# Kernel tuning notes

Hardware: AMD Instinct MI355X
Metric: run time of the kernel (lower is better)

The kernel has to match this reference:

```python
import jax, jax.numpy as jnp
import numpy as np

N = 100000   # nodes
E = 1600000  # edges (avg degree 16)
D = 64       # feature / hidden / embedding dim
OUT = 2
NEG_SLOPE = 0.2


def setup_inputs() -> dict:
    key = jax.random.key(0)
    ks = jax.random.split(key, 12)
    s = 1.0 / np.sqrt(D)
    return {
        "x": jax.random.normal(ks[0], (N, D), dtype=jnp.float32),
        "edge_index": jax.random.randint(ks[1], (2, E), 0, N, dtype=jnp.int64),
        "Wl": jax.random.normal(ks[2], (3, D, D), dtype=jnp.float32) * s,
        "bl": jnp.zeros((3, D), dtype=jnp.float32),
        "Wr": jax.random.normal(ks[3], (3, D, D), dtype=jnp.float32) * s,
        "br": jnp.zeros((3, D), dtype=jnp.float32),
        "att": jax.random.normal(ks[4], (3, D), dtype=jnp.float32) * s,
        "bg": jnp.zeros((3, D), dtype=jnp.float32),
        "Ws": jax.random.normal(ks[5], (3, D, D), dtype=jnp.float32) * s,
        "bs": jnp.zeros((3, D), dtype=jnp.float32),
        "Wout": jax.random.normal(ks[6], (D, OUT), dtype=jnp.float32) * s,
        "bout": jnp.zeros((OUT,), dtype=jnp.float32),
    }


def _gatv2(h, src, dst, Wl, bl, Wr, br, att, bg):
    # GATv2Conv (heads=1, concat, add_self_loops=False):
    #   e_ij = att . LeakyReLU(Wl h_j + Wr h_i); softmax over incoming edges of i;
    #   out_i = sum_j alpha_ij * (Wl h_j) + bias
    xl = h @ Wl + bl                      # [N, D] source transform
    xr = h @ Wr + br                      # [N, D] dest transform
    e = jax.nn.leaky_relu(xl[src] + xr[dst], NEG_SLOPE) @ att  # [E]
    m = jax.ops.segment_max(e, dst, num_segments=N)            # per-dest max
    a = jnp.exp(e - m[dst])                                    # [E]
    denom = jax.ops.segment_sum(a, dst, num_segments=N)        # [N]
    alpha = a / denom[dst]                                     # [E]
    agg = jax.ops.segment_sum(alpha[:, None] * xl[src], dst, num_segments=N)
    return agg + bg                                            # [N, D]


def reference(x, edge_index, Wl, bl, Wr, br, att, bg, Ws, bs, Wout, bout):
    src, dst = edge_index[0], edge_index[1]
    # layer 1: gat1 + skip1, relu (dropout_rate=0 -> identity)
    h = jax.nn.relu(_gatv2(x, src, dst, Wl[0], bl[0], Wr[0], br[0], att[0], bg[0])
                    + x @ Ws[0] + bs[0])
    # middle layer
    h = jax.nn.relu(_gatv2(h, src, dst, Wl[1], bl[1], Wr[1], br[1], att[1], bg[1])
                    + h @ Ws[1] + bs[1])
    # last gat layer: no relu after
    h = _gatv2(h, src, dst, Wl[2], bl[2], Wr[2], br[2], att[2], bg[2]) + h @ Ws[2] + bs[2]
    return h @ Wout + bout
```

## Files before the change

kernel.cpp:

```cpp
#include <hip/hip_runtime.h>
#include <stdint.h>

#define NN 100000
#define EE 1600000
#define DD 64
#define NBUCK 391
#define SCWG 200
#define SCCHUNK 8000

using short8 = __attribute__((ext_vector_type(8))) short;
using f32x4  = __attribute__((ext_vector_type(4))) float;
using f2     = __attribute__((ext_vector_type(2))) float;


__device__ __forceinline__ unsigned short bf16_rne(float f) {
    unsigned int u = __float_as_uint(f);
    unsigned int r = (u + 0x7FFFu + ((u >> 16) & 1u)) >> 16;
    return (unsigned short)r;
}
__device__ __forceinline__ float bf16_to_f32(unsigned short h) {
    return __uint_as_float(((unsigned int)h) << 16);
}


__global__ void bucket_hist(const int* __restrict__ dst, int* __restrict__ bhist) {
    __shared__ int h[NBUCK];
    int t = threadIdx.x;
    for (int b = t; b < NBUCK; b += 256) h[b] = 0;
    __syncthreads();
    int start = blockIdx.x * SCCHUNK;
    int endi = min(start + SCCHUNK, EE);
    for (int e = start + t; e < endi; e += 256)
        atomicAdd(&h[dst[e] >> 8], 1);
    __syncthreads();
    for (int b = t; b < NBUCK; b += 256)
        if (h[b]) atomicAdd(&bhist[b], h[b]);
}

__global__ void bucket_scan(const int* __restrict__ bhist, int* __restrict__ bbase,
                            int* __restrict__ bcursor, int* __restrict__ offsets) {
    __shared__ int s[512];
    int t = threadIdx.x;
    int v = (t < NBUCK) ? bhist[t] : 0;
    s[t] = v;
    __syncthreads();
    for (int off = 1; off < 512; off <<= 1) {
        int a = (t >= off) ? s[t - off] : 0;
        __syncthreads();
        s[t] += a;
        __syncthreads();
    }
    if (t < NBUCK) { int excl = s[t] - v; bbase[t] = excl; bcursor[t] = excl; }
    if (t == 0) { bbase[NBUCK] = EE; offsets[NN] = EE; }
}

__global__ void bucket_scatter(const int* __restrict__ src, const int* __restrict__ dst,
                               int* __restrict__ bcursor, int2* __restrict__ bedges) {
    __shared__ int cnt[NBUCK];
    __shared__ int lcur[NBUCK];
    int t = threadIdx.x;
    for (int b = t; b < NBUCK; b += 256) cnt[b] = 0;
    __syncthreads();
    int start = blockIdx.x * SCCHUNK;
    int endi = min(start + SCCHUNK, EE);
    for (int e = start + t; e < endi; e += 256)
        atomicAdd(&cnt[dst[e] >> 8], 1);
    __syncthreads();
    for (int b = t; b < NBUCK; b += 256) {
        int c = cnt[b];
        lcur[b] = c ? atomicAdd(&bcursor[b], c) : 0;
    }
    __syncthreads();
    for (int e = start + t; e < endi; e += 256) {
        int d = dst[e];
        int pos = atomicAdd(&lcur[d >> 8], 1);
        int2 v; v.x = d; v.y = src[e];
        bedges[pos] = v;
    }
}

__global__ void bucket_csr(const int2* __restrict__ bedges, const int* __restrict__ bbase,
                           int* __restrict__ offsets, int* __restrict__ csr) {
    __shared__ int ncnt[256];
    __shared__ int lofs[256];
    int b = blockIdx.x;
    int t = threadIdx.x;
    int beg = bbase[b], endb = bbase[b + 1];
    ncnt[t] = 0;
    __syncthreads();
    for (int e = beg + t; e < endb; e += 256)
        atomicAdd(&ncnt[bedges[e].x & 255], 1);
    __syncthreads();
    int v = ncnt[t];
    lofs[t] = v;
    __syncthreads();
    for (int off = 1; off < 256; off <<= 1) {
        int a = (t >= off) ? lofs[t - off] : 0;
        __syncthreads();
        lofs[t] += a;
        __syncthreads();
    }
    int excl = lofs[t] - v;
    int node = b * 256 + t;
    if (node < NN) offsets[node] = beg + excl;
    __syncthreads();
    ncnt[t] = beg + excl;
    __syncthreads();
    for (int e = beg + t; e < endb; e += 256) {
        int2 ed = bedges[e];
        int pos = atomicAdd(&ncnt[ed.x & 255], 1);
        csr[pos] = ed.y;
    }
}


__global__ void conv_w(const float* __restrict__ Wl, const float* __restrict__ Wr,
                       const float* __restrict__ Ws,
                       unsigned short* __restrict__ Wt_hi, unsigned short* __restrict__ Wt_lo) {
    int e = blockIdx.x * 256 + threadIdx.x;
    if (e >= 9 * 4096) return;
    int mat = e >> 12;
    int r   = e & 4095;
    int k   = r >> 6, n = r & 63;
    int L = mat / 3, j = mat % 3;
    const float* W = (j == 0) ? Wl : ((j == 1) ? Wr : Ws);
    float v = W[L * 4096 + k * 64 + n];
    unsigned short hi = bf16_rne(v);
    unsigned short lo = bf16_rne(v - bf16_to_f32(hi));
    Wt_hi[mat * 4096 + n * 64 + k] = hi;
    Wt_lo[mat * 4096 + n * 64 + k] = lo;
}


__global__ void conv_x(const float* __restrict__ x,
                       unsigned short* __restrict__ Ahi, unsigned short* __restrict__ Alo) {
    int i = blockIdx.x * 256 + threadIdx.x;
    int total = NN * 16;
    for (; i < total; i += gridDim.x * 256) {
        float4 v = *(const float4*)&x[(size_t)i * 4];
        ushort4 h, l;
        h.x = bf16_rne(v.x); l.x = bf16_rne(v.x - bf16_to_f32(h.x));
        h.y = bf16_rne(v.y); l.y = bf16_rne(v.y - bf16_to_f32(h.y));
        h.z = bf16_rne(v.z); l.z = bf16_rne(v.z - bf16_to_f32(h.z));
        h.w = bf16_rne(v.w); l.w = bf16_rne(v.w - bf16_to_f32(h.w));
        *(ushort4*)&Ahi[(size_t)i * 4] = h;
        *(ushort4*)&Alo[(size_t)i * 4] = l;
    }
}


__global__ __launch_bounds__(256) void gemm_mfma(
    const unsigned short* __restrict__ Ahi, const unsigned short* __restrict__ Alo,
    const unsigned short* __restrict__ Wt_hi, const unsigned short* __restrict__ Wt_lo,
    const float* __restrict__ bl, const float* __restrict__ br, const float* __restrict__ bs,
    float* __restrict__ Xl, float* __restrict__ XRS) {
    int lane = threadIdx.x & 63;
    int wid  = threadIdx.x >> 6;
    int m0 = (blockIdx.x * 4 + wid) * 16;
    if (m0 >= NN) return;

    int arow = m0 + (lane & 15);
    if (arow >= NN) arow = NN - 1;
    int koff = (lane >> 4) * 8;

    const unsigned short* abase = Ahi + (size_t)arow * 64;
    const unsigned short* lbase = Alo + (size_t)arow * 64;
    short8 ahi0 = *(const short8*)(abase + koff);
    short8 ahi1 = *(const short8*)(abase + 32 + koff);
    short8 alo0 = *(const short8*)(lbase + koff);
    short8 alo1 = *(const short8*)(lbase + 32 + koff);

    int col16 = lane & 15;
    int r0 = m0 + ((lane >> 4) << 2);

#pragma unroll
    for (int m = 0; m < 3; m++) {
        const unsigned short* wh = Wt_hi + m * 4096;
        const unsigned short* wl = Wt_lo + m * 4096;
        const float* bias = (m == 0) ? bl : ((m == 1) ? br : bs);
#pragma unroll
        for (int tt = 0; tt < 4; tt++) {
            int ncol = tt * 16 + col16;
            const unsigned short* bh = wh + ncol * 64 + koff;
            const unsigned short* blo = wl + ncol * 64 + koff;
            short8 bhi0 = *(const short8*)bh;
            short8 bhi1 = *(const short8*)(bh + 32);
            short8 blo0 = *(const short8*)blo;
            short8 blo1 = *(const short8*)(blo + 32);

            f32x4 acc = {0.f, 0.f, 0.f, 0.f};
            acc = __builtin_amdgcn_mfma_f32_16x16x32_bf16(ahi0, bhi0, acc, 0, 0, 0);
            acc = __builtin_amdgcn_mfma_f32_16x16x32_bf16(ahi1, bhi1, acc, 0, 0, 0);
            acc = __builtin_amdgcn_mfma_f32_16x16x32_bf16(ahi0, blo0, acc, 0, 0, 0);
            acc = __builtin_amdgcn_mfma_f32_16x16x32_bf16(ahi1, blo1, acc, 0, 0, 0);
            acc = __builtin_amdgcn_mfma_f32_16x16x32_bf16(alo0, bhi0, acc, 0, 0, 0);
            acc = __builtin_amdgcn_mfma_f32_16x16x32_bf16(alo1, bhi1, acc, 0, 0, 0);

            float bb = bias[ncol];
#pragma unroll
            for (int j = 0; j < 4; j++) {
                int row = r0 + j;
                if (row < NN) {
                    float v = acc[j] + bb;
                    if (m == 0)      Xl[(size_t)row * 64 + ncol]        = v;
                    else if (m == 1) XRS[(size_t)row * 128 + ncol]      = v;
                    else             XRS[(size_t)row * 128 + 64 + ncol] = v;
                }
            }
        }
    }
}


__device__ __forceinline__ float group_sum16(float t) {
    t += __int_as_float(__builtin_amdgcn_update_dpp(0, __float_as_int(t), 0xB1, 0xF, 0xF, true));
    t += __int_as_float(__builtin_amdgcn_update_dpp(0, __float_as_int(t), 0x4E, 0xF, 0xF, true));
    t += __int_as_float(__builtin_amdgcn_update_dpp(0, __float_as_int(t), 0x141, 0xF, 0xF, true));
    t += __int_as_float(__builtin_amdgcn_update_dpp(0, __float_as_int(t), 0x140, 0xF, 0xF, true));
    return t;
}

__global__ __launch_bounds__(256) void node_kernel(
    const float* __restrict__ Xl, const float* __restrict__ XRS,
    const int* __restrict__ offsets, const int* __restrict__ csr,
    const float* __restrict__ att, const float* __restrict__ bg,
    unsigned short* __restrict__ houtHi, unsigned short* __restrict__ houtLo, int do_relu,
    const float* __restrict__ Wout, const float* __restrict__ bout,
    float* __restrict__ outp, int do_out) {
    int lane = threadIdx.x & 63;
    int wid  = threadIdx.x >> 6;
    int i = blockIdx.x * 4 + wid;
    if (i >= NN) return;
    int sub = lane & 15;
    int grp = lane >> 4;

    float4 xr4  = *(const float4*)&XRS[(size_t)i * 128 + sub * 4];
    float4 att4 = *(const float4*)&att[sub * 4];
    f2 xr01 = {xr4.x, xr4.y}, xr23 = {xr4.z, xr4.w};
    f2 at01 = {att4.x, att4.y}, at23 = {att4.z, att4.w};

    f2 agg01 = {0.f, 0.f}, agg23 = {0.f, 0.f};
    float denom = 0.f;
    int beg = offsets[i], end = offsets[i + 1];

    for (int j0 = beg; j0 < end; j0 += 8) {
        int jA = j0 + grp, jB = j0 + grp + 4;
        bool vA = jA < end, vB = jB < end;
        int sA = csr[vA ? jA : beg];
        int sB = csr[vB ? jB : beg];
        float4 xA = *(const float4*)&Xl[(size_t)sA * 64 + sub * 4];
        float4 xB = *(const float4*)&Xl[(size_t)sB * 64 + sub * 4];
        f2 xA01 = {xA.x, xA.y}, xA23 = {xA.z, xA.w};
        f2 xB01 = {xB.x, xB.y}, xB23 = {xB.z, xB.w};

        f2 sA01 = xA01 + xr01;
        f2 sA23 = xA23 + xr23;
        f2 sB01 = xB01 + xr01;
        f2 sB23 = xB23 + xr23;
        f2 lA01 = { fmaxf(sA01.x, 0.2f * sA01.x), fmaxf(sA01.y, 0.2f * sA01.y) };
        f2 lA23 = { fmaxf(sA23.x, 0.2f * sA23.x), fmaxf(sA23.y, 0.2f * sA23.y) };
        f2 lB01 = { fmaxf(sB01.x, 0.2f * sB01.x), fmaxf(sB01.y, 0.2f * sB01.y) };
        f2 lB23 = { fmaxf(sB23.x, 0.2f * sB23.x), fmaxf(sB23.y, 0.2f * sB23.y) };

        f2 tAv = lA01 * at01 + lA23 * at23;
        f2 tBv = lB01 * at01 + lB23 * at23;
        float tA = group_sum16(tAv.x + tAv.y);
        float tB = group_sum16(tBv.x + tBv.y);
        float aA = vA ? __expf(tA) : 0.f;
        float aB = vB ? __expf(tB) : 0.f;

        f2 aAv = {aA, aA};
        f2 aBv = {aB, aB};
        agg01 += aAv * xA01 + aBv * xB01;
        agg23 += aAv * xA23 + aBv * xB23;
        denom += aA + aB;
    }

    float aggx = agg01.x, aggy = agg01.y, aggz = agg23.x, aggw = agg23.y;
#pragma unroll
    for (int m = 16; m <= 32; m <<= 1) {
        aggx  += __shfl_xor(aggx, m, 64);
        aggy  += __shfl_xor(aggy, m, 64);
        aggz  += __shfl_xor(aggz, m, 64);
        aggw  += __shfl_xor(aggw, m, 64);
        denom += __shfl_xor(denom, m, 64);
    }

    float inv = (denom > 0.f) ? (1.0f / denom) : 0.f;
    float4 sk4 = *(const float4*)&XRS[(size_t)i * 128 + 64 + sub * 4];
    float4 bg4 = *(const float4*)&bg[sub * 4];
    float4 res;
    res.x = aggx * inv + bg4.x + sk4.x;
    res.y = aggy * inv + bg4.y + sk4.y;
    res.z = aggz * inv + bg4.z + sk4.z;
    res.w = aggw * inv + bg4.w + sk4.w;
    if (do_relu) {
        res.x = fmaxf(res.x, 0.f); res.y = fmaxf(res.y, 0.f);
        res.z = fmaxf(res.z, 0.f); res.w = fmaxf(res.w, 0.f);
    }
    if (do_out) {
        float4 w01 = *(const float4*)&Wout[8 * sub];
        float4 w23 = *(const float4*)&Wout[8 * sub + 4];
        float o0 = res.x * w01.x + res.y * w01.z + res.z * w23.x + res.w * w23.z;
        float o1 = res.x * w01.y + res.y * w01.w + res.z * w23.y + res.w * w23.w;
        o0 = group_sum16(o0);
        o1 = group_sum16(o1);
        if (lane == 0) {
            outp[(size_t)i * 2 + 0] = o0 + bout[0];
            outp[(size_t)i * 2 + 1] = o1 + bout[1];
        }
    } else {
        if (grp == 0) {
            ushort4 h, l;
            h.x = bf16_rne(res.x); l.x = bf16_rne(res.x - bf16_to_f32(h.x));
            h.y = bf16_rne(res.y); l.y = bf16_rne(res.y - bf16_to_f32(h.y));
            h.z = bf16_rne(res.z); l.z = bf16_rne(res.z - bf16_to_f32(h.z));
            h.w = bf16_rne(res.w); l.w = bf16_rne(res.w - bf16_to_f32(h.w));
            *(ushort4*)&houtHi[(size_t)i * 64 + sub * 4] = h;
            *(ushort4*)&houtLo[(size_t)i * 64 + sub * 4] = l;
        }
    }
}


extern "C" void kernel_launch(void* const* d_in, const int* in_sizes, int n_in,
                              void* d_out, int out_size, void* d_ws, size_t ws_size,
                              hipStream_t stream) {
    const float* x    = (const float*)d_in[0];
    const int*   ei   = (const int*)d_in[1];
    const float* Wl   = (const float*)d_in[2];
    const float* bl   = (const float*)d_in[3];
    const float* Wr   = (const float*)d_in[4];
    const float* br   = (const float*)d_in[5];
    const float* att  = (const float*)d_in[6];
    const float* bg   = (const float*)d_in[7];
    const float* Ws   = (const float*)d_in[8];
    const float* bs   = (const float*)d_in[9];
    const float* Wout = (const float*)d_in[10];
    const float* bout = (const float*)d_in[11];
    float* out = (float*)d_out;

    size_t off = 0;
    char* base = (char*)d_ws;
    auto alloc = [&](size_t bytes) -> void* {
        void* p = base + off;
        off += (bytes + 255) & ~(size_t)255;
        return p;
    };
    float* Xl   = (float*)alloc((size_t)NN * 64 * 4);
    float* XRS  = (float*)alloc((size_t)NN * 128 * 4);
    unsigned short* Ahi = (unsigned short*)alloc((size_t)NN * 64 * 2);
    unsigned short* Alo = (unsigned short*)alloc((size_t)NN * 64 * 2);
    unsigned short* Bhi = (unsigned short*)alloc((size_t)NN * 64 * 2);
    unsigned short* Blo = (unsigned short*)alloc((size_t)NN * 64 * 2);
    unsigned short* Wthi = (unsigned short*)alloc((size_t)9 * 4096 * 2);
    unsigned short* Wtlo = (unsigned short*)alloc((size_t)9 * 4096 * 2);
    int*  bhist  = (int*)alloc((size_t)NBUCK * 4);
    int*  bbase  = (int*)alloc((size_t)(NBUCK + 1) * 4);
    int*  bcur   = (int*)alloc((size_t)NBUCK * 4);
    int2* bedges = (int2*)alloc((size_t)EE * 8);
    int*  offs   = (int*)alloc((size_t)(NN + 1) * 4);
    int*  csr    = (int*)alloc((size_t)EE * 4);

    const int* src = ei;
    const int* dst = ei + EE;

    hipMemsetAsync(bhist, 0, (size_t)NBUCK * 4, stream);
    bucket_hist<<<SCWG, 256, 0, stream>>>(dst, bhist);
    bucket_scan<<<1, 512, 0, stream>>>(bhist, bbase, bcur, offs);
    bucket_scatter<<<SCWG, 256, 0, stream>>>(src, dst, bcur, bedges);
    bucket_csr<<<NBUCK, 256, 0, stream>>>(bedges, bbase, offs, csr);

    conv_w<<<(9 * 4096 + 255) / 256, 256, 0, stream>>>(Wl, Wr, Ws, Wthi, Wtlo);
    conv_x<<<2048, 256, 0, stream>>>(x, Ahi, Alo);

    unsigned short* curHi = Ahi; unsigned short* curLo = Alo;
    unsigned short* nxtHi = Bhi; unsigned short* nxtLo = Blo;
    for (int L = 0; L < 3; L++) {
        gemm_mfma<<<(NN + 63) / 64, 256, 0, stream>>>(
            curHi, curLo, Wthi + (size_t)L * 3 * 4096, Wtlo + (size_t)L * 3 * 4096,
            bl + L * 64, br + L * 64, bs + L * 64, Xl, XRS);
        node_kernel<<<NN / 4, 256, 0, stream>>>(
            Xl, XRS, offs, csr, att + L * 64, bg + L * 64,
            nxtHi, nxtLo, (L < 2) ? 1 : 0,
            Wout, bout, out, (L == 2) ? 1 : 0);
        unsigned short* th = curHi; curHi = nxtHi; nxtHi = th;
        unsigned short* tl = curLo; curLo = nxtLo; nxtLo = tl;
    }
}
```

Before: 413.2 us.

## Store gathered source features as bf16 and pack bucket edges into 32 bits

The Xl source-transform output that every edge gathers is now stored as bf16 instead of fp32, which halves the bytes of the random gather in the node kernel. The bucketed edge array used to build the CSR now packs the low 8 bits of the destination and a 24-bit source index into one 32-bit word instead of an int2, halving that scratch traffic. The risks are lower precision in the attention logits and aggregated messages, and the packing relies on node ids fitting in 24 bits.

```diff
diff --git a/kernel.cpp b/kernel.cpp
--- a/kernel.cpp
+++ b/kernel.cpp
@@ -55,7 +55,7 @@
 }
 
 __global__ void bucket_scatter(const int* __restrict__ src, const int* __restrict__ dst,
-                               int* __restrict__ bcursor, int2* __restrict__ bedges) {
+                               int* __restrict__ bcursor, unsigned int* __restrict__ bedges) {
     __shared__ int cnt[NBUCK];
     __shared__ int lcur[NBUCK];
     int t = threadIdx.x;
@@ -74,12 +74,11 @@
     for (int e = start + t; e < endi; e += 256) {
         int d = dst[e];
         int pos = atomicAdd(&lcur[d >> 8], 1);
-        int2 v; v.x = d; v.y = src[e];
-        bedges[pos] = v;
-    }
-}
-
-__global__ void bucket_csr(const int2* __restrict__ bedges, const int* __restrict__ bbase,
+        bedges[pos] = ((unsigned int)(d & 255) << 24) | (unsigned int)src[e];
+    }
+}
+
+__global__ void bucket_csr(const unsigned int* __restrict__ bedges, const int* __restrict__ bbase,
                            int* __restrict__ offsets, int* __restrict__ csr) {
     __shared__ int ncnt[256];
     __shared__ int lofs[256];
@@ -89,7 +88,7 @@
     ncnt[t] = 0;
     __syncthreads();
     for (int e = beg + t; e < endb; e += 256)
-        atomicAdd(&ncnt[bedges[e].x & 255], 1);
+        atomicAdd(&ncnt[bedges[e] >> 24], 1);
     __syncthreads();
     int v = ncnt[t];
     lofs[t] = v;
@@ -107,9 +106,9 @@
     ncnt[t] = beg + excl;
     __syncthreads();
     for (int e = beg + t; e < endb; e += 256) {
-        int2 ed = bedges[e];
-        int pos = atomicAdd(&ncnt[ed.x & 255], 1);
-        csr[pos] = ed.y;
+        unsigned int ed = bedges[e];
+        int pos = atomicAdd(&ncnt[ed >> 24], 1);
+        csr[pos] = (int)(ed & 0xFFFFFFu);
     }
 }
 
@@ -153,7 +152,7 @@
     const unsigned short* __restrict__ Ahi, const unsigned short* __restrict__ Alo,
     const unsigned short* __restrict__ Wt_hi, const unsigned short* __restrict__ Wt_lo,
     const float* __restrict__ bl, const float* __restrict__ br, const float* __restrict__ bs,
-    float* __restrict__ Xl, float* __restrict__ XRS) {
+    unsigned short* __restrict__ Xlb, float* __restrict__ XRS) {
     int lane = threadIdx.x & 63;
     int wid  = threadIdx.x >> 6;
     int m0 = (blockIdx.x * 4 + wid) * 16;
@@ -202,7 +201,7 @@
                 int row = r0 + j;
                 if (row < NN) {
                     float v = acc[j] + bb;
-                    if (m == 0)      Xl[(size_t)row * 64 + ncol]        = v;
+                    if (m == 0)      Xlb[(size_t)row * 64 + ncol]       = bf16_rne(v);
                     else if (m == 1) XRS[(size_t)row * 128 + ncol]      = v;
                     else             XRS[(size_t)row * 128 + 64 + ncol] = v;
                 }
@@ -221,7 +220,7 @@
 }
 
 __global__ __launch_bounds__(256) void node_kernel(
-    const float* __restrict__ Xl, const float* __restrict__ XRS,
+    const unsigned short* __restrict__ Xlb, const float* __restrict__ XRS,
     const int* __restrict__ offsets, const int* __restrict__ csr,
     const float* __restrict__ att, const float* __restrict__ bg,
     unsigned short* __restrict__ houtHi, unsigned short* __restrict__ houtLo, int do_relu,
@@ -248,10 +247,12 @@
         bool vA = jA < end, vB = jB < end;
         int sA = csr[vA ? jA : beg];
         int sB = csr[vB ? jB : beg];
-        float4 xA = *(const float4*)&Xl[(size_t)sA * 64 + sub * 4];
-        float4 xB = *(const float4*)&Xl[(size_t)sB * 64 + sub * 4];
-        f2 xA01 = {xA.x, xA.y}, xA23 = {xA.z, xA.w};
-        f2 xB01 = {xB.x, xB.y}, xB23 = {xB.z, xB.w};
+        uint2 uA = *(const uint2*)&Xlb[(size_t)sA * 64 + sub * 4];
+        uint2 uB = *(const uint2*)&Xlb[(size_t)sB * 64 + sub * 4];
+        f2 xA01 = { __uint_as_float(uA.x << 16), __uint_as_float(uA.x & 0xFFFF0000u) };
+        f2 xA23 = { __uint_as_float(uA.y << 16), __uint_as_float(uA.y & 0xFFFF0000u) };
+        f2 xB01 = { __uint_as_float(uB.x << 16), __uint_as_float(uB.x & 0xFFFF0000u) };
+        f2 xB23 = { __uint_as_float(uB.y << 16), __uint_as_float(uB.y & 0xFFFF0000u) };
 
         f2 sA01 = xA01 + xr01;
         f2 sA23 = xA23 + xr23;
@@ -347,7 +348,7 @@
         off += (bytes + 255) & ~(size_t)255;
         return p;
     };
-    float* Xl   = (float*)alloc((size_t)NN * 64 * 4);
+    unsigned short* Xlb = (unsigned short*)alloc((size_t)NN * 64 * 2);
     float* XRS  = (float*)alloc((size_t)NN * 128 * 4);
     unsigned short* Ahi = (unsigned short*)alloc((size_t)NN * 64 * 2);
     unsigned short* Alo = (unsigned short*)alloc((size_t)NN * 64 * 2);
@@ -358,7 +359,7 @@
     int*  bhist  = (int*)alloc((size_t)NBUCK * 4);
     int*  bbase  = (int*)alloc((size_t)(NBUCK + 1) * 4);
     int*  bcur   = (int*)alloc((size_t)NBUCK * 4);
-    int2* bedges = (int2*)alloc((size_t)EE * 8);
+    unsigned int* bedges = (unsigned int*)alloc((size_t)EE * 4);
     int*  offs   = (int*)alloc((size_t)(NN + 1) * 4);
     int*  csr    = (int*)alloc((size_t)EE * 4);
 
@@ -379,9 +380,9 @@
     for (int L = 0; L < 3; L++) {
         gemm_mfma<<<(NN + 63) / 64, 256, 0, stream>>>(
             curHi, curLo, Wthi + (size_t)L * 3 * 4096, Wtlo + (size_t)L * 3 * 4096,
-            bl + L * 64, br + L * 64, bs + L * 64, Xl, XRS);
+            bl + L * 64, br + L * 64, bs + L * 64, Xlb, XRS);
         node_kernel<<<NN / 4, 256, 0, stream>>>(
-            Xl, XRS, offs, csr, att + L * 64, bg + L * 64,
+            Xlb, XRS, offs, csr, att + L * 64, bg + L * 64,
             nxtHi, nxtLo, (L < 2) ? 1 : 0,
             Wout, bout, out, (L == 2) ? 1 : 0);
         unsigned short* th = curHi; curHi = nxtHi; nxtHi = th;
```

After: 382.2 us. 1.08x faster.
